# Optimization experiments

Hardware: AMD Instinct MI355X
Metric: run time of the kernel (lower is better)

Reference implementation:

```python
import jax, jax.numpy as jnp
import numpy as np

N = 100000
E = 1600000
F = 64
OUT = 7

def setup_inputs() -> dict:
    key = jax.random.key(0)
    k1, k2, k3, k4, k5 = jax.random.split(key, 5)
    x = jax.random.normal(k1, (N, F), dtype=jnp.float32)
    edge_index = jax.random.randint(k2, (2, E), 0, N, dtype=jnp.int64)
    W_l = jax.random.normal(k3, (F, OUT), dtype=jnp.float32) / np.sqrt(F)
    b_l = jax.random.normal(k4, (OUT,), dtype=jnp.float32) * 0.01
    W_r = jax.random.normal(k5, (F, OUT), dtype=jnp.float32) / np.sqrt(F)
    return {"x": x, "edge_index": edge_index, "W_l": W_l, "b_l": b_l, "W_r": W_r}

def reference(x, edge_index, W_l, b_l, W_r):
    # PyG SAGEConv (mean aggr): out = lin_l(mean_{j in N(i)} x_j) + lin_r(x_i), then relu
    src, dst = edge_index[0], edge_index[1]
    msgs = x[src]                                            # [E, F] gather
    agg = jax.ops.segment_sum(msgs, dst, num_segments=N)     # [N, F]
    cnt = jax.ops.segment_sum(jnp.ones((E,), dtype=x.dtype), dst, num_segments=N)
    mean = agg / jnp.maximum(cnt, 1.0)[:, None]              # isolated nodes -> 0
    out = mean @ W_l + b_l + x @ W_r                         # [N, 7]
    return jax.nn.relu(out)
```

## Files before the change

### kernel.cpp

```cpp
#include <hip/hip_runtime.h>

#define NN 100000
#define NE 1600000
#define FIN 64
#define FOUT 7

#define BSH 9
#define BMASK 511u
#define NB  196
#define CAP 9216
#define PBLK 512
#define PTH  512
#define EPB (NE / PBLK)
#define EPT ((EPB + PTH - 1) / PTH)
#define ATH 1024
#define APT ((CAP + ATH - 1) / ATH)

__device__ __forceinline__ unsigned bf16r(float f) {
    unsigned u = __float_as_uint(f);
    return (u + 0x7fffu + ((u >> 16) & 1u)) >> 16;
}
__device__ __forceinline__ float bflo(unsigned u) { return __uint_as_float(u << 16); }
__device__ __forceinline__ float bfhi(unsigned u) { return __uint_as_float(u & 0xffff0000u); }

__global__ __launch_bounds__(256) void proj_kernel(
    const float* __restrict__ x, const float* __restrict__ Wl,
    const float* __restrict__ bl, const float* __restrict__ Wr,
    unsigned* __restrict__ z, float* __restrict__ outself, int n)
{
    int i = blockIdx.x * blockDim.x + threadIdx.x;
    if (i >= n) return;

    float al[FOUT], ar[FOUT];
#pragma unroll
    for (int j = 0; j < FOUT; ++j) { al[j] = 0.f; ar[j] = 0.f; }

    const float4* xr = (const float4*)(x + (size_t)i * FIN);
#pragma unroll
    for (int kk = 0; kk < FIN / 4; ++kk) {
        float4 xv = xr[kk];
        float v[4] = {xv.x, xv.y, xv.z, xv.w};
#pragma unroll
        for (int c = 0; c < 4; ++c) {
            int k = kk * 4 + c;
#pragma unroll
            for (int j = 0; j < FOUT; ++j) {
                al[j] = fmaf(v[c], Wl[k * FOUT + j], al[j]);
                ar[j] = fmaf(v[c], Wr[k * FOUT + j], ar[j]);
            }
        }
    }

    uint4 pk;
    pk.x = bf16r(al[0]) | (bf16r(al[1]) << 16);
    pk.y = bf16r(al[2]) | (bf16r(al[3]) << 16);
    pk.z = bf16r(al[4]) | (bf16r(al[5]) << 16);
    pk.w = bf16r(al[6]);
    ((uint4*)z)[i] = pk;

    float* o = outself + (size_t)i * FOUT;
#pragma unroll
    for (int j = 0; j < FOUT; ++j)
        o[j] = ar[j] + bl[j];
}

__global__ __launch_bounds__(PTH) void part_kernel(
    const int* __restrict__ eg, int* __restrict__ gcur,
    unsigned* __restrict__ part)
{
    __shared__ unsigned st_rank[NB];
    __shared__ unsigned st_scan[256];
    __shared__ unsigned st_start[NB];
    __shared__ unsigned st_gbase[NB];
    __shared__ unsigned stage[EPB];
    __shared__ unsigned char bof[EPB];

    const int t  = threadIdx.x;
    const int e0 = blockIdx.x * EPB;

    for (int b = t; b < NB; b += PTH) st_rank[b] = 0;
    __syncthreads();

    unsigned held[EPT], hbr[EPT];
    int nh = 0;
#pragma unroll
    for (int j = 0; j < EPT; ++j) {
        int k = t + j * PTH;
        if (k < EPB) {
            unsigned s = (unsigned)eg[e0 + k];
            unsigned d = (unsigned)eg[NE + e0 + k];
            unsigned b = d >> BSH;
            unsigned r = atomicAdd(&st_rank[b], 1u);
            held[nh] = ((d & BMASK) << 17) | s;
            hbr[nh]  = (b << 16) | r;
            ++nh;
        }
    }
    __syncthreads();

    if (t < 256) st_scan[t] = (t < NB) ? st_rank[t] : 0u;
    __syncthreads();
    for (int off = 1; off < 256; off <<= 1) {
        unsigned v = 0;
        if (t < 256 && t >= off) v = st_scan[t - off];
        __syncthreads();
        if (t < 256) st_scan[t] += v;
        __syncthreads();
    }
    if (t < NB) {
        unsigned cnt = st_rank[t];
        st_start[t] = st_scan[t] - cnt;
        st_gbase[t] = cnt ? (unsigned)atomicAdd(&gcur[t], (int)cnt) : 0u;
    }
    __syncthreads();

    for (int j = 0; j < nh; ++j) {
        unsigned b = hbr[j] >> 16, r = hbr[j] & 0xffffu;
        unsigned pos = st_start[b] + r;
        stage[pos] = held[j];
        bof[pos]   = (unsigned char)b;
    }
    __syncthreads();

    for (int j = t; j < EPB; j += PTH) {
        unsigned b = bof[j];
        unsigned idx = st_gbase[b] + (unsigned)j - st_start[b];
        if (idx < CAP) part[(size_t)b * CAP + idx] = stage[j];
    }
}

__global__ __launch_bounds__(ATH) void acc_kernel(
    const int* __restrict__ gcur, const unsigned* __restrict__ part,
    const unsigned* __restrict__ zb, float* __restrict__ out)
{
    __shared__ unsigned s_cnt[512];
    __shared__ unsigned s_scan[512];
    __shared__ unsigned sstage[CAP];
    __shared__ float    lacc[512 * 8];

    const int t = threadIdx.x;
    const int b = blockIdx.x;

    if (t < 512) s_cnt[t] = 0;
    __syncthreads();

    int cnt = gcur[b];
    if (cnt > CAP) cnt = CAP;
    const unsigned* ep = part + (size_t)b * CAP;

    unsigned hsrc[APT], hnr[APT];
    int nh = 0;
#pragma unroll
    for (int j = 0; j < APT; ++j) {
        int k = t + j * ATH;
        if (k < cnt) {
            unsigned e = ep[k];
            unsigned node = e >> 17;
            unsigned r = atomicAdd(&s_cnt[node], 1u);
            hsrc[nh] = e & 0x1FFFFu;
            hnr[nh]  = (node << 16) | r;
            ++nh;
        }
    }
    __syncthreads();

    if (t < 512) s_scan[t] = s_cnt[t];
    __syncthreads();
    for (int off = 1; off < 512; off <<= 1) {
        unsigned v = 0;
        if (t < 512 && t >= off) v = s_scan[t - off];
        __syncthreads();
        if (t < 512) s_scan[t] += v;
        __syncthreads();
    }
    __syncthreads();

    for (int j = 0; j < nh; ++j) {
        unsigned node = hnr[j] >> 16, r = hnr[j] & 0xffffu;
        sstage[(s_scan[node] - s_cnt[node]) + r] = hsrc[j];
    }
    __syncthreads();

    unsigned node = t & 511u;
    unsigned half = t >> 9;
    unsigned deg  = s_cnt[node];
    unsigned base = s_scan[node] - deg;
    unsigned lo = half ? (deg >> 1) : 0u;
    unsigned hi = half ? deg : (deg >> 1);

    float a0 = 0.f, a1 = 0.f, a2 = 0.f, a3 = 0.f, a4 = 0.f, a5 = 0.f, a6 = 0.f;
    for (unsigned j = lo; j < hi; ++j) {
        unsigned src = sstage[base + j];
        uint4 zr = ((const uint4*)zb)[src];
        a0 += bflo(zr.x); a1 += bfhi(zr.x);
        a2 += bflo(zr.y); a3 += bfhi(zr.y);
        a4 += bflo(zr.z); a5 += bfhi(zr.z);
        a6 += bflo(zr.w);
    }

    if (half) {
        float* L = &lacc[node * 8];
        *(float4*)(L)     = make_float4(a0, a1, a2, a3);
        *(float4*)(L + 4) = make_float4(a4, a5, a6, 0.f);
    }
    __syncthreads();

    if (!half) {
        const float* L = &lacc[node * 8];
        a0 += L[0]; a1 += L[1]; a2 += L[2]; a3 += L[3];
        a4 += L[4]; a5 += L[5]; a6 += L[6];
        int i = (b << BSH) + (int)node;
        if (i < NN) {
            float r = 1.0f / (float)max((int)deg, 1);
            float* o = out + (size_t)i * FOUT;
            o[0] = fmaxf(fmaf(a0, r, o[0]), 0.f);
            o[1] = fmaxf(fmaf(a1, r, o[1]), 0.f);
            o[2] = fmaxf(fmaf(a2, r, o[2]), 0.f);
            o[3] = fmaxf(fmaf(a3, r, o[3]), 0.f);
            o[4] = fmaxf(fmaf(a4, r, o[4]), 0.f);
            o[5] = fmaxf(fmaf(a5, r, o[5]), 0.f);
            o[6] = fmaxf(fmaf(a6, r, o[6]), 0.f);
        }
    }
}

extern "C" void kernel_launch(void* const* d_in, const int* in_sizes, int n_in,
                              void* d_out, int out_size, void* d_ws, size_t ws_size,
                              hipStream_t stream) {
    const float* x   = (const float*)d_in[0];
    const int*   edg = (const int*)d_in[1];
    const float* Wl  = (const float*)d_in[2];
    const float* bl  = (const float*)d_in[3];
    const float* Wr  = (const float*)d_in[4];
    float* out = (float*)d_out;

    unsigned* z    = (unsigned*)d_ws;
    unsigned* part = z + (size_t)NN * 4;
    int*      gcur = (int*)(part + (size_t)NB * CAP);

    hipMemsetAsync(gcur, 0, NB * sizeof(int), stream);

    proj_kernel<<<(NN + 255) / 256, 256, 0, stream>>>(x, Wl, bl, Wr, z, out, NN);
    part_kernel<<<PBLK, PTH, 0, stream>>>(edg, gcur, part);
    acc_kernel<<<NB, ATH, 0, stream>>>(gcur, part, z, out);
}
```

Measured before the change: 127.9 us.

## Fuse projection into partition kernel and shrink destination buckets to 128 nodes

Merges the node projection and the edge partition kernels into one launch, with extra blocks doing the projection so both phases run concurrently. Destination buckets shrink from 512 to 128 nodes, giving 782 accumulate blocks of 256 threads instead of 196 blocks of 1024. The Hillis-Steele shared-memory scans are replaced by wavefront shuffle scans. The aim is better occupancy, load balance and fewer barriers, at the cost of more global atomics on the bucket counters and a tighter per-bucket capacity (2560) that could overflow on skewed inputs.

```diff
diff --git a/kernel.cpp b/kernel.cpp
--- a/kernel.cpp
+++ b/kernel.cpp
@@ -5,16 +5,17 @@
 #define FIN 64
 #define FOUT 7
 
-#define BSH 9
-#define BMASK 511u
-#define NB  196
-#define CAP 9216
+#define BSH 7
+#define NBK 782
+#define CAP 2560
 #define PBLK 512
 #define PTH  512
 #define EPB (NE / PBLK)
-#define EPT ((EPB + PTH - 1) / PTH)
-#define ATH 1024
-#define APT ((CAP + ATH - 1) / ATH)
+#define EPT 7
+#define PROJB 196
+#define ATH 256
+#define APT 10
+#define INVALID 0xFFFFFFFFu
 
 __device__ __forceinline__ unsigned bf16r(float f) {
     unsigned u = __float_as_uint(f);
@@ -23,66 +24,66 @@
 __device__ __forceinline__ float bflo(unsigned u) { return __uint_as_float(u << 16); }
 __device__ __forceinline__ float bfhi(unsigned u) { return __uint_as_float(u & 0xffff0000u); }
 
-__global__ __launch_bounds__(256) void proj_kernel(
+__global__ __launch_bounds__(512) void part_proj_kernel(
+    const int* __restrict__ eg,
     const float* __restrict__ x, const float* __restrict__ Wl,
     const float* __restrict__ bl, const float* __restrict__ Wr,
-    unsigned* __restrict__ z, float* __restrict__ outself, int n)
+    int* __restrict__ gcur, unsigned* __restrict__ part,
+    unsigned* __restrict__ z, float* __restrict__ outself)
 {
-    int i = blockIdx.x * blockDim.x + threadIdx.x;
-    if (i >= n) return;
-
-    float al[FOUT], ar[FOUT];
-#pragma unroll
-    for (int j = 0; j < FOUT; ++j) { al[j] = 0.f; ar[j] = 0.f; }
-
-    const float4* xr = (const float4*)(x + (size_t)i * FIN);
-#pragma unroll
-    for (int kk = 0; kk < FIN / 4; ++kk) {
-        float4 xv = xr[kk];
-        float v[4] = {xv.x, xv.y, xv.z, xv.w};
-#pragma unroll
-        for (int c = 0; c < 4; ++c) {
-            int k = kk * 4 + c;
-#pragma unroll
-            for (int j = 0; j < FOUT; ++j) {
-                al[j] = fmaf(v[c], Wl[k * FOUT + j], al[j]);
-                ar[j] = fmaf(v[c], Wr[k * FOUT + j], ar[j]);
+    __shared__ unsigned st_rank[NBK];
+    __shared__ unsigned st_start[NBK];
+    __shared__ unsigned st_gbase[NBK];
+    __shared__ unsigned wtot[8];
+    __shared__ unsigned stage[EPB];
+    __shared__ unsigned short bof[EPB];
+
+    const int t = threadIdx.x;
+
+    if (blockIdx.x >= PBLK) {
+        int i = (blockIdx.x - PBLK) * 512 + t;
+        if (i >= NN) return;
+
+        float al[FOUT], ar[FOUT];
+#pragma unroll
+        for (int j = 0; j < FOUT; ++j) { al[j] = 0.f; ar[j] = 0.f; }
+
+        const float4* xr = (const float4*)(x + (size_t)i * FIN);
+#pragma unroll
+        for (int kk = 0; kk < FIN / 4; ++kk) {
+            float4 xv = xr[kk];
+            float v[4] = {xv.x, xv.y, xv.z, xv.w};
+#pragma unroll
+            for (int c = 0; c < 4; ++c) {
+                int k = kk * 4 + c;
+#pragma unroll
+                for (int j = 0; j < FOUT; ++j) {
+                    al[j] = fmaf(v[c], Wl[k * FOUT + j], al[j]);
+                    ar[j] = fmaf(v[c], Wr[k * FOUT + j], ar[j]);
+                }
             }
         }
-    }
-
-    uint4 pk;
-    pk.x = bf16r(al[0]) | (bf16r(al[1]) << 16);
-    pk.y = bf16r(al[2]) | (bf16r(al[3]) << 16);
-    pk.z = bf16r(al[4]) | (bf16r(al[5]) << 16);
-    pk.w = bf16r(al[6]);
-    ((uint4*)z)[i] = pk;
-
-    float* o = outself + (size_t)i * FOUT;
-#pragma unroll
-    for (int j = 0; j < FOUT; ++j)
-        o[j] = ar[j] + bl[j];
-}
-
-__global__ __launch_bounds__(PTH) void part_kernel(
-    const int* __restrict__ eg, int* __restrict__ gcur,
-    unsigned* __restrict__ part)
-{
-    __shared__ unsigned st_rank[NB];
-    __shared__ unsigned st_scan[256];
-    __shared__ unsigned st_start[NB];
-    __shared__ unsigned st_gbase[NB];
-    __shared__ unsigned stage[EPB];
-    __shared__ unsigned char bof[EPB];
-
-    const int t  = threadIdx.x;
+
+        uint4 pk;
+        pk.x = bf16r(al[0]) | (bf16r(al[1]) << 16);
+        pk.y = bf16r(al[2]) | (bf16r(al[3]) << 16);
+        pk.z = bf16r(al[4]) | (bf16r(al[5]) << 16);
+        pk.w = bf16r(al[6]);
+        ((uint4*)z)[i] = pk;
+
+        float* o = outself + (size_t)i * FOUT;
+#pragma unroll
+        for (int j = 0; j < FOUT; ++j)
+            o[j] = ar[j] + bl[j];
+        return;
+    }
+
     const int e0 = blockIdx.x * EPB;
 
-    for (int b = t; b < NB; b += PTH) st_rank[b] = 0;
+    for (int b = t; b < NBK; b += PTH) st_rank[b] = 0;
     __syncthreads();
 
     unsigned held[EPT], hbr[EPT];
-    int nh = 0;
 #pragma unroll
     for (int j = 0; j < EPT; ++j) {
         int k = t + j * PTH;
@@ -91,34 +92,51 @@
             unsigned d = (unsigned)eg[NE + e0 + k];
             unsigned b = d >> BSH;
             unsigned r = atomicAdd(&st_rank[b], 1u);
-            held[nh] = ((d & BMASK) << 17) | s;
-            hbr[nh]  = (b << 16) | r;
-            ++nh;
-        }
-    }
-    __syncthreads();
-
-    if (t < 256) st_scan[t] = (t < NB) ? st_rank[t] : 0u;
-    __syncthreads();
-    for (int off = 1; off < 256; off <<= 1) {
-        unsigned v = 0;
-        if (t < 256 && t >= off) v = st_scan[t - off];
+            held[j] = ((d & 127u) << 17) | s;
+            hbr[j]  = (b << 12) | r;
+        } else hbr[j] = INVALID;
+    }
+    __syncthreads();
+
+    {
+        int lane = t & 63, wv = t >> 6;
+        unsigned i0 = 2 * t, i1 = 2 * t + 1;
+        unsigned c0 = (i0 < NBK) ? st_rank[i0] : 0u;
+        unsigned c1 = (i1 < NBK) ? st_rank[i1] : 0u;
+        unsigned p = c0 + c1, s = p;
+#pragma unroll
+        for (int off = 1; off < 64; off <<= 1) {
+            unsigned v = (unsigned)__shfl_up((int)s, off, 64);
+            if (lane >= off) s += v;
+        }
+        if (lane == 63) wtot[wv] = s;
         __syncthreads();
-        if (t < 256) st_scan[t] += v;
+        if (t == 0) {
+            unsigned run = 0;
+#pragma unroll
+            for (int w = 0; w < 8; ++w) { unsigned tmp = wtot[w]; wtot[w] = run; run += tmp; }
+        }
         __syncthreads();
-    }
-    if (t < NB) {
-        unsigned cnt = st_rank[t];
-        st_start[t] = st_scan[t] - cnt;
-        st_gbase[t] = cnt ? (unsigned)atomicAdd(&gcur[t], (int)cnt) : 0u;
-    }
-    __syncthreads();
-
-    for (int j = 0; j < nh; ++j) {
-        unsigned b = hbr[j] >> 16, r = hbr[j] & 0xffffu;
-        unsigned pos = st_start[b] + r;
-        stage[pos] = held[j];
-        bof[pos]   = (unsigned char)b;
+        unsigned S = s + wtot[wv];
+        if (i0 < NBK) {
+            st_start[i0] = S - p;
+            if (c0) st_gbase[i0] = (unsigned)atomicAdd(&gcur[i0], (int)c0);
+        }
+        if (i1 < NBK) {
+            st_start[i1] = S - c1;
+            if (c1) st_gbase[i1] = (unsigned)atomicAdd(&gcur[i1], (int)c1);
+        }
+    }
+    __syncthreads();
+
+#pragma unroll
+    for (int j = 0; j < EPT; ++j) {
+        if (hbr[j] != INVALID) {
+            unsigned b = hbr[j] >> 12, r = hbr[j] & 0xfffu;
+            unsigned pos = st_start[b] + r;
+            stage[pos] = held[j];
+            bof[pos]   = (unsigned short)b;
+        }
     }
     __syncthreads();
 
@@ -133,15 +151,15 @@
     const int* __restrict__ gcur, const unsigned* __restrict__ part,
     const unsigned* __restrict__ zb, float* __restrict__ out)
 {
-    __shared__ unsigned s_cnt[512];
-    __shared__ unsigned s_scan[512];
+    __shared__ unsigned s_cnt[128];
+    __shared__ unsigned s_start[128];
     __shared__ unsigned sstage[CAP];
-    __shared__ float    lacc[512 * 8];
+    __shared__ float    lacc[128 * 8];
 
     const int t = threadIdx.x;
     const int b = blockIdx.x;
 
-    if (t < 512) s_cnt[t] = 0;
+    if (t < 128) s_cnt[t] = 0;
     __syncthreads();
 
     int cnt = gcur[b];
@@ -149,7 +167,6 @@
     const unsigned* ep = part + (size_t)b * CAP;
 
     unsigned hsrc[APT], hnr[APT];
-    int nh = 0;
 #pragma unroll
     for (int j = 0; j < APT; ++j) {
         int k = t + j * ATH;
@@ -157,34 +174,38 @@
             unsigned e = ep[k];
             unsigned node = e >> 17;
             unsigned r = atomicAdd(&s_cnt[node], 1u);
-            hsrc[nh] = e & 0x1FFFFu;
-            hnr[nh]  = (node << 16) | r;
-            ++nh;
-        }
-    }
-    __syncthreads();
-
-    if (t < 512) s_scan[t] = s_cnt[t];
-    __syncthreads();
-    for (int off = 1; off < 512; off <<= 1) {
-        unsigned v = 0;
-        if (t < 512 && t >= off) v = s_scan[t - off];
-        __syncthreads();
-        if (t < 512) s_scan[t] += v;
-        __syncthreads();
-    }
-    __syncthreads();
-
-    for (int j = 0; j < nh; ++j) {
-        unsigned node = hnr[j] >> 16, r = hnr[j] & 0xffffu;
-        sstage[(s_scan[node] - s_cnt[node]) + r] = hsrc[j];
-    }
-    __syncthreads();
-
-    unsigned node = t & 511u;
-    unsigned half = t >> 9;
+            hsrc[j] = e & 0x1FFFFu;
+            hnr[j]  = (node << 12) | r;
+        } else hnr[j] = INVALID;
+    }
+    __syncthreads();
+
+    if (t < 64) {
+        unsigned c0 = s_cnt[2 * t], c1 = s_cnt[2 * t + 1];
+        unsigned p = c0 + c1, s = p;
+#pragma unroll
+        for (int off = 1; off < 64; off <<= 1) {
+            unsigned v = (unsigned)__shfl_up((int)s, off, 64);
+            if ((t & 63) >= off) s += v;
+        }
+        s_start[2 * t]     = s - p;
+        s_start[2 * t + 1] = s - c1;
+    }
+    __syncthreads();
+
+#pragma unroll
+    for (int j = 0; j < APT; ++j) {
+        if (hnr[j] != INVALID) {
+            unsigned node = hnr[j] >> 12, r = hnr[j] & 0xfffu;
+            sstage[s_start[node] + r] = hsrc[j];
+        }
+    }
+    __syncthreads();
+
+    unsigned node = t & 127u;
+    unsigned half = t >> 7;
     unsigned deg  = s_cnt[node];
-    unsigned base = s_scan[node] - deg;
+    unsigned base = s_start[node];
     unsigned lo = half ? (deg >> 1) : 0u;
     unsigned hi = half ? deg : (deg >> 1);
 
@@ -236,11 +257,11 @@
 
     unsigned* z    = (unsigned*)d_ws;
     unsigned* part = z + (size_t)NN * 4;
-    int*      gcur = (int*)(part + (size_t)NB * CAP);
-
-    hipMemsetAsync(gcur, 0, NB * sizeof(int), stream);
-
-    proj_kernel<<<(NN + 255) / 256, 256, 0, stream>>>(x, Wl, bl, Wr, z, out, NN);
-    part_kernel<<<PBLK, PTH, 0, stream>>>(edg, gcur, part);
-    acc_kernel<<<NB, ATH, 0, stream>>>(gcur, part, z, out);
-}
+    int*      gcur = (int*)(part + (size_t)NBK * CAP);
+
+    hipMemsetAsync(gcur, 0, NBK * sizeof(int), stream);
+
+    part_proj_kernel<<<PBLK + PROJB, 512, 0, stream>>>(edg, x, Wl, bl, Wr,
+                                                       gcur, part, z, out);
+    acc_kernel<<<NBK, ATH, 0, stream>>>(gcur, part, z, out);
+}
```

Result: slower. 142.7 us (+11.6%).
